# Kernel optimization log

Measured on AMD Instinct MI355X. Metric: run time of the kernel, lower is better.

The kernel has to match this reference:

```python
import jax, jax.numpy as jnp
from jax import lax
import numpy as np

INPUT_DIM = 1024; ENT_DIM = 256; KEY_DIM = 32; FUNC_DIM = 256; HID = 32
NUM_LAYERS = 1; UNIT_TYPE_DIM = 259; MAX_ENT = 64; B = 256; N = 512
NEG = 1e9

def _ln(x, g, b, eps=1e-5):
    m = x.mean(-1, keepdims=True)
    v = ((x - m) ** 2).mean(-1, keepdims=True)
    return (x - m) / jnp.sqrt(v + eps) * g + b

def setup_inputs() -> dict:
    key = jax.random.key(0)
    ks = jax.random.split(key, 16)
    def lin(k, i, o, s=0.02):
        return jax.random.normal(k, (i, o), jnp.float32) * s, jnp.zeros((o,), jnp.float32)
    p = {}
    p['key_fc_w'], p['key_fc_b'] = lin(ks[0], ENT_DIM, KEY_DIM)
    p['func_fc_w'], p['func_fc_b'] = lin(ks[1], UNIT_TYPE_DIM, FUNC_DIM)
    p['fc1_w'], p['fc1_b'] = lin(ks[2], INPUT_DIM, FUNC_DIM)
    p['fc2_w'], p['fc2_b'] = lin(ks[3], FUNC_DIM, KEY_DIM)
    p['embed_fc_w'], p['embed_fc_b'] = lin(ks[4], KEY_DIM, INPUT_DIM)
    p['lstm_wx'] = jax.random.normal(ks[5], (NUM_LAYERS, KEY_DIM, 4 * HID), jnp.float32) * 0.05
    p['lstm_wh'] = jax.random.normal(ks[6], (NUM_LAYERS, HID, 4 * HID), jnp.float32) * 0.05
    p['lstm_b'] = jnp.zeros((NUM_LAYERS, 4 * HID), jnp.float32)
    p['lstm_ln_gx'] = jnp.ones((NUM_LAYERS, 4 * HID), jnp.float32)
    p['lstm_ln_bx'] = jnp.zeros((NUM_LAYERS, 4 * HID), jnp.float32)
    p['lstm_ln_gh'] = jnp.ones((NUM_LAYERS, 4 * HID), jnp.float32)
    p['lstm_ln_bh'] = jnp.zeros((NUM_LAYERS, 4 * HID), jnp.float32)
    inp = {
        'embedding': jax.random.normal(ks[7], (B, INPUT_DIM), jnp.float32),
        'available_unit_type_mask': (jax.random.uniform(ks[8], (B, UNIT_TYPE_DIM)) < 0.5).astype(jnp.float32),
        'available_units_mask': jnp.ones((B, N), jnp.float32),
        'entity_embedding': jax.random.normal(ks[9], (B, N, ENT_DIM), jnp.float32),
        'temperature': jnp.float32(1.0),
    }
    inp.update(p)
    return inp

def reference(embedding, available_unit_type_mask, available_units_mask, entity_embedding,
              temperature, key_fc_w, key_fc_b, func_fc_w, func_fc_b, fc1_w, fc1_b,
              fc2_w, fc2_b, embed_fc_w, embed_fc_b, lstm_wx, lstm_wh, lstm_b,
              lstm_ln_gx, lstm_ln_bx, lstm_ln_gh, lstm_ln_bh):
    relu = jax.nn.relu
    # _get_key: [B,N,KEY] + end-flag row of zeros -> [B,N+1,KEY]
    key = entity_embedding @ key_fc_w + key_fc_b
    key = jnp.concatenate([key, jnp.zeros((B, 1, KEY_DIM), key.dtype)], axis=1)
    end_idx = N
    # _get_init_query
    func_embed = relu(available_unit_type_mask @ func_fc_w + func_fc_b)
    x0 = relu(embedding @ fc1_w + fc1_b)
    x0 = relu((x0 + func_embed) @ fc2_w + fc2_b)  # [B, KEY_DIM]
    mask0 = jnp.concatenate([available_units_mask, jnp.ones((B, 1), available_units_mask.dtype)], axis=1)

    h0 = jnp.zeros((NUM_LAYERS, B, HID), key.dtype)
    c0 = jnp.zeros((NUM_LAYERS, B, HID), key.dtype)
    units0 = jnp.zeros((B, N + 1), jnp.int32)
    done0 = jnp.zeros((B,), bool)
    rng0 = jax.random.key(42)

    def step(carry, _):
        x, h, c, mask, units, done, rng = carry
        xi = x
        hs, cs = [], []
        for l in range(NUM_LAYERS):  # LN-LSTM, gate order i,f,o,u (DI-engine)
            gate = (_ln(xi @ lstm_wx[l], lstm_ln_gx[l], lstm_ln_bx[l])
                    + _ln(h[l] @ lstm_wh[l], lstm_ln_gh[l], lstm_ln_bh[l]) + lstm_b[l])
            i_g, f_g, o_g, u_g = jnp.split(gate, 4, axis=-1)
            cl = jax.nn.sigmoid(f_g) * c[l] + jax.nn.sigmoid(i_g) * jnp.tanh(u_g)
            hl = jax.nn.sigmoid(o_g) * jnp.tanh(cl)
            hs.append(hl); cs.append(cl); xi = hl
        h_new = jnp.stack(hs); c_new = jnp.stack(cs)
        q = (xi[:, None, :] * key).mean(-1)          # [B, N+1] pointer scores
        q = q - (1.0 - mask) * NEG
        rng, sk = jax.random.split(rng)
        idx = jax.random.categorical(sk, q / temperature, axis=-1)  # [B]
        is_end = idx == end_idx
        active = jnp.logical_not(done)
        sel = active & jnp.logical_not(is_end)
        onehot = jax.nn.one_hot(idx, N + 1, dtype=mask.dtype)
        units = jnp.where(sel[:, None] & (onehot > 0.5), 1, units)
        mask = jnp.where(sel[:, None], mask * (1.0 - onehot), mask)
        done = done | (active & is_end)
        return (xi, h_new, c_new, mask, units, done, rng), (q, active)

    carry, (logits, valid) = lax.scan(step, (x0, h0, c0, mask0, units0, done0, rng0), None, length=MAX_ENT)
    units = carry[4]
    emb_sel = (units[..., None].astype(key.dtype) * key).mean(axis=1)  # [B, KEY_DIM]
    emb_sel = emb_sel @ embed_fc_w + embed_fc_b
    return logits, valid, units, embedding + emb_sel
```

## Files before the change

kernel.cpp:

```cpp
#include <hip/hip_runtime.h>
#include <stdint.h>
#include <stddef.h>

#define JAX_PARTITIONABLE 1

#define B_   256
#define N_   512
#define NP_  513
#define KROW 516
#define T_   64
#define CS   4
#define NCH  16
#define NEGC 1e9f

__host__ __device__ __forceinline__ void tf2x32(uint32_t k0, uint32_t k1,
    uint32_t x0, uint32_t x1, uint32_t& o0, uint32_t& o1) {
  const uint32_t k2 = k0 ^ k1 ^ 0x1BD11BDAu;
#define TFR(r) { x0 += x1; x1 = (x1 << (r)) | (x1 >> (32 - (r))); x1 ^= x0; }
  x0 += k0; x1 += k1;
  TFR(13) TFR(15) TFR(26) TFR(6)
  x0 += k1; x1 += k2 + 1u;
  TFR(17) TFR(29) TFR(16) TFR(24)
  x0 += k2; x1 += k0 + 2u;
  TFR(13) TFR(15) TFR(26) TFR(6)
// ... 1 lines not shown
  TFR(17) TFR(29) TFR(16) TFR(24)
  x0 += k1; x1 += k2 + 4u;
  TFR(13) TFR(15) TFR(26) TFR(6)
  x0 += k2; x1 += k0 + 5u;
#undef TFR
  o0 = x0; o1 = x1;
}

struct SkKeys { uint32_t k[128]; };

static SkKeys compute_chain() {
  SkKeys s;
  uint32_t r0 = 0u, r1 = 42u;
  for (int t = 0; t < 64; ++t) {
#if JAX_PARTITIONABLE
    uint32_t a0, a1, b0, b1;
    tf2x32(r0, r1, 0u, 0u, a0, a1);
    tf2x32(r0, r1, 0u, 1u, b0, b1);
    s.k[2*t] = b0; s.k[2*t+1] = b1;
    r0 = a0; r1 = a1;
#else
    uint32_t p0, p1, q0, q1;
    tf2x32(r0, r1, 0u, 2u, p0, p1);
    tf2x32(r0, r1, 1u, 3u, q0, q1);
    s.k[2*t] = p1; s.k[2*t+1] = q1;
    r0 = p0; r1 = q0;
#endif
  }
  return s;
}

__device__ __forceinline__ float gumbel_draw(uint32_t k0, uint32_t k1, int b, int n) {
  uint32_t bits;
#if JAX_PARTITIONABLE
  uint32_t j = (uint32_t)(b * NP_ + n);
  uint32_t o0, o1; tf2x32(k0, k1, 0u, j, o0, o1);
  bits = o0 ^ o1;
#else
  int j = b * NP_ + n;
  uint32_t o0, o1;
  if (j < 65664) { tf2x32(k0, k1, (uint32_t)j, (uint32_t)(j + 65664), o0, o1); bits = o0; }
  else           { tf2x32(k0, k1, (uint32_t)(j - 65664), (uint32_t)j, o0, o1); bits = o1; }
#endif
  float f = __uint_as_float((bits >> 9) | 0x3F800000u) - 1.0f;
  const float TINY = 1.17549435e-38f;
  float u = fmaxf(TINY, f + TINY);
  return -logf(-logf(u));
}

__device__ __forceinline__ float sigm(float x) {
  return 0.5f + 0.5f * tanhf(0.5f * x);
}

__device__ __forceinline__ void bar_lds() {
  asm volatile("s_waitcnt lgkmcnt(0)\n\ts_barrier" ::: "memory");
}

#define OFF_KEY   0
#define OFF_H     16512
#define OFF_Q     18560
#define OFF_G     22688
#define OFF_UNITS 33008
#define OFF_SK    33524
#define OFF_ES    33652
#define OFF_PART  33684
#define OFF_T     34196
#define OFF_X0    34452
#define LDS_FLOATS 34484

__global__ void __launch_bounds__(512, 2)
suh_fused(const float* __restrict__ emb, const float* __restrict__ autm,
          const float* __restrict__ aum, const float* __restrict__ ent,
          const float* __restrict__ temp_p,
          const float* __restrict__ key_w, const float* __restrict__ key_b,
          const float* __restrict__ func_w, const float* __restrict__ func_b,
          const float* __restrict__ fc1_w, const float* __restrict__ fc1_b,
          const float* __restrict__ fc2_w, const float* __restrict__ fc2_b,
          const float* __restrict__ emb_w, const float* __restrict__ emb_b,
          const float* __restrict__ wx, const float* __restrict__ wh,
          const float* __restrict__ lstm_bb,
          const float* __restrict__ ln_gx, const float* __restrict__ ln_bx,
          const float* __restrict__ ln_gh, const float* __restrict__ ln_bh,
          float* __restrict__ out_logits, float* __restrict__ out_valid,
          float* __restrict__ out_units, float* __restrict__ out_final,
          SkKeys sk)
{
  extern __shared__ __align__(16) float sm[];
  int* smi = (int*)sm;
  const int b   = blockIdx.x;
  const int tid = threadIdx.x;
  const int L   = tid - 64;

  const float temp = temp_p[0];

  if (tid < 256) {
    float a = 0.f;
    const float* e = emb + (size_t)b * 1024;
    #pragma unroll 8
    for (int k = 0; k < 1024; ++k) a += e[k] * fc1_w[k * 256 + tid];
    a = fmaxf(a + fc1_b[tid], 0.f);
    float f = 0.f;
    const float* m = autm + (size_t)b * 259;
    for (int k = 0; k < 259; ++k) f += m[k] * func_w[k * 256 + tid];
    f = fmaxf(f + func_b[tid], 0.f);
    sm[OFF_T + tid] = a + f;
  } else {
    if (tid < 384) smi[OFF_SK + (tid - 256)] = (int)sk.k[tid - 256];
    if (tid >= 480) sm[OFF_KEY + (tid - 480) * KROW + N_] = 0.f;
  }
  __syncthreads();

  if (tid < 32) {
    float s = 0.f;
    #pragma unroll 8
    for (int m2 = 0; m2 < 256; ++m2) s += sm[OFF_T + m2] * fc2_w[m2 * 32 + tid];
    sm[OFF_X0 + tid] = fmaxf(s + fc2_b[tid], 0.f);
  }
  __syncthreads();

  float kr0[32], kr1[32];
  float mreg[8], ureg[8];
  float m512 = 1.0f;
  int done_reg = 0;

  auto qprep = [&](int cc, int qs) {
    const int qb = OFF_Q + qs * (CS * 516);
    #pragma unroll 1
    for (int tl = 0; tl < CS; ++tl) {
      const int hb = OFF_H + (cc * CS + tl) * 32;
      float hv[32];
      #pragma unroll
      for (int r = 0; r < 8; ++r) {
        float4 v = *(const float4*)&sm[hb + r * 4];
        hv[r*4] = v.x; hv[r*4+1] = v.y; hv[r*4+2] = v.z; hv[r*4+3] = v.w;
      }
      float a0 = 0.f;
      #pragma unroll
      for (int k = 0; k < 32; ++k) a0 += hv[k] * kr0[k];
      sm[qb + tl * 516 + L] = a0 * (1.0f / 32.0f);
      if (L < 64) {
        float a1 = 0.f;
        #pragma unroll
        for (int k = 0; k < 32; ++k) a1 += hv[k] * kr1[k];
        sm[qb + tl * 516 + L + 448] = a1 * (1.0f / 32.0f);
      }
    }
  };
  auto gprep = [&](int cc, int gs) {
    const int gb = OFF_G + gs * (CS * 516);
    #pragma unroll 1
    for (int i = 0; i < 5; ++i) {
      const int idx = i * 448 + L;
      if (idx < CS * 512) {
        const int tl = idx >> 9, n = idx & 511;
        const int t = cc * CS + tl;
        sm[gb + tl * 516 + n] =
            gumbel_draw((uint32_t)smi[OFF_SK + 2*t], (uint32_t)smi[OFF_SK + 2*t + 1], b, n);
      }
    }
    if (L < CS) {
      const int t = cc * CS + L;
      sm[gb + L * 516 + N_] =
          gumbel_draw((uint32_t)smi[OFF_SK + 2*t], (uint32_t)smi[OFF_SK + 2*t + 1], b, N_);
    }
  };

  if (tid < 64) {
    float wxr0[32], wxr1[32], whr0[32], whr1[32];
    #pragma unroll
    for (int k = 0; k < 32; ++k) {
      wxr0[k] = wx[k * 128 + tid];
      wxr1[k] = wx[k * 128 + 64 + tid];
      whr0[k] = wh[k * 128 + tid];
      whr1[k] = wh[k * 128 + 64 + tid];
    }
    #pragma unroll
    for (int k = 0; k < 32; ++k) {
      asm volatile("" : "+v"(wxr0[k]), "+v"(wxr1[k]), "+v"(whr0[k]), "+v"(whr1[k]));
    }
    const float gxg0 = ln_gx[tid], gxg1 = ln_gx[tid + 64];
    const float gxb0 = ln_bx[tid], gxb1 = ln_bx[tid + 64];
    const float ghg0 = ln_gh[tid], ghg1 = ln_gh[tid + 64];
    const float ghb0 = ln_bh[tid], ghb1 = ln_bh[tid + 64];
    const float lb0  = lstm_bb[tid], lb1 = lstm_bb[tid + 64];

    float xf[32];
    #pragma unroll
    for (int r = 0; r < 8; ++r) {
      float4 v = *(const float4*)&sm[OFF_X0 + r * 4];
      xf[r*4] = v.x; xf[r*4+1] = v.y; xf[r*4+2] = v.z; xf[r*4+3] = v.w;
    }
    float creg = 0.f;

    #pragma unroll 1
    for (int t = 0; t < T_; ++t) {
      float a0 = 0.f, a1 = 0.f, b0 = 0.f, b1 = 0.f;
      #pragma unroll
      for (int k = 0; k < 32; ++k) { a0 += xf[k] * wxr0[k]; a1 += xf[k] * wxr1[k]; }
      if (t > 0) {
        #pragma unroll
        for (int k = 0; k < 32; ++k) { b0 += xf[k] * whr0[k]; b1 += xf[k] * whr1[k]; }
      }
      float sx = a0 + a1, sh = b0 + b1;
      for (int off = 32; off; off >>= 1) {
        sx += __shfl_down(sx, off);
        sh += __shfl_down(sh, off);
      }
      float mx  = __shfl(sx, 0) * (1.0f / 128.0f);
      float mh2 = __shfl(sh, 0) * (1.0f / 128.0f);
      float dx0 = a0 - mx, dx1 = a1 - mx;
      float dh0 = b0 - mh2, dh1 = b1 - mh2;
      float ssx = dx0 * dx0 + dx1 * dx1;
      float ssh = dh0 * dh0 + dh1 * dh1;
      for (int off = 32; off; off >>= 1) {
        ssx += __shfl_down(ssx, off);
        ssh += __shfl_down(ssh, off);
      }
      float vx = __shfl(ssx, 0) * (1.0f / 128.0f);
      float vh = __shfl(ssh, 0) * (1.0f / 128.0f);
      float rx = 1.0f / sqrtf(vx + 1e-5f);
      float rh = 1.0f / sqrtf(vh + 1e-5f);
      float lnx0 = dx0 * rx * gxg0 + gxb0;
      float lnx1 = dx1 * rx * gxg1 + gxb1;
      float lnh0 = dh0 * rh * ghg0 + ghb0;
      float lnh1 = dh1 * rh * ghg1 + ghb1;
      float g0 = lnx0 + lnh0 + lb0;
      float g1 = lnx1 + lnh1 + lb1;
      float fq = __shfl(g0, tid + 32);
      float uq = __shfl(g1, tid + 32);
      float cN = sigm(fq) * creg + sigm(g0) * tanhf(uq);
      float hN = sigm(g1) * tanhf(cN);
      creg = cN;
      if (tid < 32) sm[OFF_H + t * 32 + tid] = hN;
      #pragma unroll
      for (int k = 0; k < 32; ++k) xf[k] = __shfl(hN, k);
    }
  } else {
    const float4* kw4 = (const float4*)key_w;
    {
      const float4* er = (const float4*)(ent + ((size_t)b * N_ + L) * 256);
      float acc[32];
      #pragma unroll
      for (int c = 0; c < 32; ++c) acc[c] = 0.f;
      #pragma unroll 1
      for (int k4 = 0; k4 < 64; ++k4) {
        float4 ev = er[k4];
        float e4[4] = {ev.x, ev.y, ev.z, ev.w};
        #pragma unroll
        for (int j = 0; j < 4; ++j) {
          const int k = k4 * 4 + j;
          #pragma unroll
          for (int c4 = 0; c4 < 8; ++c4) {
            float4 w = kw4[k * 8 + c4];
            acc[c4*4+0] += e4[j] * w.x;
            acc[c4*4+1] += e4[j] * w.y;
            acc[c4*4+2] += e4[j] * w.z;
            acc[c4*4+3] += e4[j] * w.w;
          }
        }
      }
      #pragma unroll
      for (int c = 0; c < 32; ++c) {
        kr0[c] = acc[c] + key_b[c];
        sm[OFF_KEY + c * KROW + L] = kr0[c];
      }
    }
    if (L < 64) {
      const int n = L + 448;
      const float4* er = (const float4*)(ent + ((size_t)b * N_ + n) * 256);
      float acc[32];
      #pragma unroll
      for (int c = 0; c < 32; ++c) acc[c] = 0.f;
      #pragma unroll 1
      for (int k4 = 0; k4 < 64; ++k4) {
        float4 ev = er[k4];
        float e4[4] = {ev.x, ev.y, ev.z, ev.w};
        #pragma unroll
        for (int j = 0; j < 4; ++j) {
          const int k = k4 * 4 + j;
          #pragma unroll
          for (int c4 = 0; c4 < 8; ++c4) {
            float4 w = kw4[k * 8 + c4];
            acc[c4*4+0] += e4[j] * w.x;
            acc[c4*4+1] += e4[j] * w.y;
            acc[c4*4+2] += e4[j] * w.z;
            acc[c4*4+3] += e4[j] * w.w;
          }
        }
      }
      #pragma unroll
      for (int c = 0; c < 32; ++c) {
        kr1[c] = acc[c] + key_b[c];
        sm[OFF_KEY + c * KROW + n] = kr1[c];
      }
    }
    #pragma unroll
    for (int k = 0; k < 32; ++k) {
      asm volatile("" : "+v"(kr0[k]), "+v"(kr1[k]));
    }
    #pragma unroll 1
    for (int cc = 0; cc < 4; ++cc) gprep(cc, cc);
  }
  __syncthreads();

  if (tid < 64) {
    #pragma unroll
    for (int j = 0; j < 8; ++j) {
      mreg[j] = aum[(size_t)b * N_ + tid + 64 * j];
      ureg[j] = 0.f;
    }
  } else {
    qprep(0, 0);
  }
  bar_lds();

  for (int c = 0; c < NCH; ++c) {
    if (tid < 64) {
      const int qbase = OFF_Q + (c & 1) * (CS * 516);
      const int gbase = OFF_G + (c % 5) * (CS * 516);
      #pragma unroll 1
      for (int tl = 0; tl < CS; ++tl) {
        const int t = c * CS + tl;
        float* lrow = out_logits + ((size_t)t * B_ + b) * NP_;
        float bv = 0.f; int bi = 0;
        #pragma unroll
        for (int j = 0; j < 8; ++j) {
          const int n = tid + 64 * j;
          float q = sm[qbase + tl * 516 + n] - (1.0f - mreg[j]) * NEGC;
          lrow[n] = q;
          float v = q / temp + sm[gbase + tl * 516 + n];
          if (j == 0) { bv = v; bi = n; }
          else if (v > bv) { bv = v; bi = n; }
        }
        if (tid == 0) {
          float q = -(1.0f - m512) * NEGC;
          lrow[N_] = q;
          float v = q / temp + sm[gbase + tl * 516 + N_];
          if (v > bv) { bv = v; bi = N_; }
        }
        for (int off = 32; off; off >>= 1) {
          float ov = __shfl_down(bv, off);
          int   oi = __shfl_down(bi, off);
          if (ov > bv || (ov == bv && oi < bi)) { bv = ov; bi = oi; }
        }
        const int sel_i = __shfl(bi, 0);
        const int active = !done_reg;
        const int is_end = (sel_i == N_);
        if (tid == 0) out_valid[(size_t)t * B_ + b] = active ? 1.0f : 0.0f;
        if (active && !is_end) {
          #pragma unroll
          for (int j = 0; j < 8; ++j)
            if (tid + 64 * j == sel_i) { mreg[j] = 0.0f; ureg[j] = 1.0f; }
        }
        if (active && is_end) done_reg = 1;
      }
    } else {
      if (c + 1 < NCH) qprep(c + 1, (c + 1) & 1);
      if (c + 4 < NCH) gprep(c + 4, (c + 4) % 5);
    }
    bar_lds();
  }

  if (tid < 64) {
    #pragma unroll
    for (int j = 0; j < 8; ++j) sm[OFF_UNITS + tid + 64 * j] = ureg[j];
    if (tid == 0) sm[OFF_UNITS + N_] = 0.f;
  }
  __syncthreads();

  {
    const int g = tid >> 5, cc = tid & 31;
    float p = 0.f;
    const int n0 = g * 32;
    for (int nn = 0; nn < 32; ++nn) {
      const int n = n0 + nn;
      p += sm[OFF_UNITS + n] * sm[OFF_KEY + cc * KROW + n];
    }
    if (g == 15) p += sm[OFF_UNITS + N_] * sm[OFF_KEY + cc * KROW + N_];
    sm[OFF_PART + g * 32 + cc] = p;
  }
  for (int n = tid; n < NP_; n += 512) out_units[(size_t)b * NP_ + n] = sm[OFF_UNITS + n];
  __syncthreads();
  if (tid < 32) {
    float s = 0.f;
    #pragma unroll
    for (int g = 0; g < 16; ++g) s += sm[OFF_PART + g * 32 + tid];
    sm[OFF_ES + tid] = s / 513.0f;
  }
  __syncthreads();
  {
    const float* e = emb + (size_t)b * 1024;
    for (int d = tid; d < 1024; d += 512) {
      float a = 0.f;
      #pragma unroll
      for (int k = 0; k < 32; ++k) a += sm[OFF_ES + k] * emb_w[k * 1024 + d];
      out_final[(size_t)b * 1024 + d] = e[d] + a + emb_b[d];
    }
  }
}

extern "C" void kernel_launch(void* const* d_in, const int* in_sizes, int n_in,
                              void* d_out, int out_size, void* d_ws, size_t ws_size,
                              hipStream_t stream) {
  (void)in_sizes; (void)n_in; (void)d_ws; (void)ws_size; (void)out_size;
  const float* emb    = (const float*)d_in[0];
  const float* autm   = (const float*)d_in[1];
  const float* aum    = (const float*)d_in[2];
  const float* ent    = (const float*)d_in[3];
  const float* temp   = (const float*)d_in[4];
  const float* key_w  = (const float*)d_in[5];
  const float* key_b  = (const float*)d_in[6];
  const float* func_w = (const float*)d_in[7];
  const float* func_b = (const float*)d_in[8];
  const float* fc1_w  = (const float*)d_in[9];
  const float* fc1_b  = (const float*)d_in[10];
  const float* fc2_w  = (const float*)d_in[11];
  const float* fc2_b  = (const float*)d_in[12];
  const float* emb_w  = (const float*)d_in[13];
  const float* emb_b  = (const float*)d_in[14];
// ... 22 lines not shown
```

Baseline: 242.4 us.

## Split LSTM across two waves with LDS flags and overlap prologue work

Restructures the prologue so the LSTM recurrence is split between two wavefronts: one computes the input-side projection and gate update, the other the recurrent-side projection and layernorm, synchronised through LDS flag spin-waits. The fc1/func MLP, key projection across 256 threads, and gumbel pre-generation now run concurrently instead of in barrier-separated phases. The gumbel ring buffer shrinks from 5 to 3 slots to cut LDS use, and key rows are reloaded from LDS into registers after the barrier. This adds spin-wait handshakes per timestep and a less deep gumbel prefetch in exchange for shortening the serial prologue.

After: 246.7 us. Within noise of the previous version (+1.8%).

```diff
diff --git a/kernel.cpp b/kernel.cpp
--- a/kernel.cpp
+++ b/kernel.cpp
@@ -80,18 +80,24 @@
 __device__ __forceinline__ void bar_lds() {
   asm volatile("s_waitcnt lgkmcnt(0)\n\ts_barrier" ::: "memory");
 }
+__device__ __forceinline__ void lds_fence() {
+  asm volatile("s_waitcnt lgkmcnt(0)" ::: "memory");
+}
 
 #define OFF_KEY   0
 #define OFF_H     16512
 #define OFF_Q     18560
 #define OFF_G     22688
-#define OFF_UNITS 33008
-#define OFF_SK    33524
-#define OFF_ES    33652
-#define OFF_PART  33684
-#define OFF_T     34196
-#define OFF_X0    34452
-#define LDS_FLOATS 34484
+#define OFF_UNITS 28880
+#define OFF_LNH   29396
+#define OFF_T     29524
+#define OFF_X0    29780
+#define OFF_ES    29812
+#define OFF_PART  29844
+#define OFF_FLAGA 30356
+#define OFF_FLAGB 30420
+#define OFF_CTRT  30484
+#define LDS_FLOATS 30488
 
 __global__ void __launch_bounds__(512, 2)
 suh_fused(const float* __restrict__ emb, const float* __restrict__ autm,
@@ -112,35 +118,16 @@
 {
   extern __shared__ __align__(16) float sm[];
   int* smi = (int*)sm;
+  volatile int* vsmi = (volatile int*)sm;
   const int b   = blockIdx.x;
   const int tid = threadIdx.x;
   const int L   = tid - 64;
 
   const float temp = temp_p[0];
 
-  if (tid < 256) {
-    float a = 0.f;
-    const float* e = emb + (size_t)b * 1024;
-    #pragma unroll 8
-    for (int k = 0; k < 1024; ++k) a += e[k] * fc1_w[k * 256 + tid];
-    a = fmaxf(a + fc1_b[tid], 0.f);
-    float f = 0.f;
-    const float* m = autm + (size_t)b * 259;
-    for (int k = 0; k < 259; ++k) f += m[k] * func_w[k * 256 + tid];
-    f = fmaxf(f + func_b[tid], 0.f);
-    sm[OFF_T + tid] = a + f;
-  } else {
-    if (tid < 384) smi[OFF_SK + (tid - 256)] = (int)sk.k[tid - 256];
-    if (tid >= 480) sm[OFF_KEY + (tid - 480) * KROW + N_] = 0.f;
-  }
-  __syncthreads();
-
-  if (tid < 32) {
-    float s = 0.f;
-    #pragma unroll 8
-    for (int m2 = 0; m2 < 256; ++m2) s += sm[OFF_T + m2] * fc2_w[m2 * 32 + tid];
-    sm[OFF_X0 + tid] = fmaxf(s + fc2_b[tid], 0.f);
-  }
+  if (tid < 64)        smi[OFF_FLAGB + tid] = 0;
+  else if (tid < 128)  smi[OFF_FLAGA + (tid - 64)] = 0;
+  else if (tid == 128) smi[OFF_CTRT] = 0;
   __syncthreads();
 
   float kr0[32], kr1[32];
@@ -148,126 +135,151 @@
   float m512 = 1.0f;
   int done_reg = 0;
 
-  auto qprep = [&](int cc, int qs) {
-    const int qb = OFF_Q + qs * (CS * 516);
+  if (tid < 256) {
+    {
+      float a = 0.f;
+      const float* e = emb + (size_t)b * 1024;
+      #pragma unroll 8
+      for (int k = 0; k < 1024; ++k) a += e[k] * fc1_w[k * 256 + tid];
+      a = fmaxf(a + fc1_b[tid], 0.f);
+      float f = 0.f;
+      const float* m = autm + (size_t)b * 259;
+      for (int k = 0; k < 259; ++k) f += m[k] * func_w[k * 256 + tid];
+      f = fmaxf(f + func_b[tid], 0.f);
+      sm[OFF_T + tid] = a + f;
+    }
+    lds_fence();
+    if ((tid & 63) == 0) atomicAdd(&smi[OFF_CTRT], 1);
+
+    if (tid < 64) {
+      while (vsmi[OFF_CTRT] != 4) __builtin_amdgcn_s_sleep(1);
+      if (tid < 32) {
+        float s = 0.f;
+        #pragma unroll 8
+        for (int m2 = 0; m2 < 256; ++m2) s += sm[OFF_T + m2] * fc2_w[m2 * 32 + tid];
+        sm[OFF_X0 + tid] = fmaxf(s + fc2_b[tid], 0.f);
+      }
+      float wxr0[32], wxr1[32];
+      #pragma unroll
+      for (int k = 0; k < 32; ++k) {
+        wxr0[k] = wx[k * 128 + tid];
+        wxr1[k] = wx[k * 128 + 64 + tid];
+      }
+      #pragma unroll
+      for (int k = 0; k < 32; ++k) asm volatile("" : "+v"(wxr0[k]), "+v"(wxr1[k]));
+      const float gxg0 = ln_gx[tid], gxg1 = ln_gx[tid + 64];
+      const float gxb0 = ln_bx[tid], gxb1 = ln_bx[tid + 64];
+      const float lb0  = lstm_bb[tid], lb1 = lstm_bb[tid + 64];
+
+      float xf[32];
+      #pragma unroll
+      for (int r = 0; r < 8; ++r) {
+        float4 v = *(const float4*)&sm[OFF_X0 + r * 4];
+        xf[r*4] = v.x; xf[r*4+1] = v.y; xf[r*4+2] = v.z; xf[r*4+3] = v.w;
+      }
+      float creg = 0.f;
+
+      #pragma unroll 1
+      for (int t = 0; t < T_; ++t) {
+        float a0 = 0.f, a1 = 0.f;
+        #pragma unroll
+        for (int k = 0; k < 32; ++k) { a0 += xf[k] * wxr0[k]; a1 += xf[k] * wxr1[k]; }
+        float sx = a0 + a1;
+        for (int off = 32; off; off >>= 1) sx += __shfl_down(sx, off);
+        float mx = __shfl(sx, 0) * (1.0f / 128.0f);
+        float dx0 = a0 - mx, dx1 = a1 - mx;
+        float ssx = dx0 * dx0 + dx1 * dx1;
+        for (int off = 32; off; off >>= 1) ssx += __shfl_down(ssx, off);
+        float vx = __shfl(ssx, 0) * (1.0f / 128.0f);
+        float rx = 1.0f / sqrtf(vx + 1e-5f);
+        float lnx0 = dx0 * rx * gxg0 + gxb0;
+        float lnx1 = dx1 * rx * gxg1 + gxb1;
+        while (vsmi[OFF_FLAGA + t] == 0) __builtin_amdgcn_s_sleep(1);
+        float lnh0 = sm[OFF_LNH + tid];
+        float lnh1 = sm[OFF_LNH + 64 + tid];
+        float g0 = lnx0 + lnh0 + lb0;
+        float g1 = lnx1 + lnh1 + lb1;
+        float fq = __shfl(g0, tid + 32);
+        float uq = __shfl(g1, tid + 32);
+        float cN = sigm(fq) * creg + sigm(g0) * tanhf(uq);
+        float hN = sigm(g1) * tanhf(cN);
+        creg = cN;
+        if (tid < 32) sm[OFF_H + t * 32 + tid] = hN;
+        lds_fence();
+        if (tid == 0) smi[OFF_FLAGB + t] = 1;
+        #pragma unroll
+        for (int k = 0; k < 32; ++k) xf[k] = __shfl(hN, k);
+      }
+    } else if (tid < 128) {
+      const int l = tid - 64;
+      float whr0[32], whr1[32];
+      #pragma unroll
+      for (int k = 0; k < 32; ++k) {
+        whr0[k] = wh[k * 128 + l];
+        whr1[k] = wh[k * 128 + 64 + l];
+      }
+      #pragma unroll
+      for (int k = 0; k < 32; ++k) asm volatile("" : "+v"(whr0[k]), "+v"(whr1[k]));
+      const float ghg0 = ln_gh[l], ghg1 = ln_gh[l + 64];
+      const float ghb0 = ln_bh[l], ghb1 = ln_bh[l + 64];
+
+      #pragma unroll 1
+      for (int t = 0; t < T_; ++t) {
+        float b0 = 0.f, b1 = 0.f;
+        if (t > 0) {
+          while (vsmi[OFF_FLAGB + (t - 1)] == 0) __builtin_amdgcn_s_sleep(1);
+          float hr[32];
+          #pragma unroll
+          for (int r = 0; r < 8; ++r) {
+            float4 v = *(const float4*)&sm[OFF_H + (t - 1) * 32 + r * 4];
+            hr[r*4] = v.x; hr[r*4+1] = v.y; hr[r*4+2] = v.z; hr[r*4+3] = v.w;
+          }
+          #pragma unroll
+          for (int k = 0; k < 32; ++k) { b0 += hr[k] * whr0[k]; b1 += hr[k] * whr1[k]; }
+        }
+        float sh = b0 + b1;
+        for (int off = 32; off; off >>= 1) sh += __shfl_down(sh, off);
+        float mh2 = __shfl(sh, 0) * (1.0f / 128.0f);
+        float dh0 = b0 - mh2, dh1 = b1 - mh2;
+        float ssh = dh0 * dh0 + dh1 * dh1;
+        for (int off = 32; off; off >>= 1) ssh += __shfl_down(ssh, off);
+        float vh = __shfl(ssh, 0) * (1.0f / 128.0f);
+        float rh = 1.0f / sqrtf(vh + 1e-5f);
+        sm[OFF_LNH + l]      = dh0 * rh * ghg0 + ghb0;
+        sm[OFF_LNH + 64 + l] = dh1 * rh * ghg1 + ghb1;
+        lds_fence();
+        if (l == 0) smi[OFF_FLAGA + t] = 1;
+      }
+    } else {
+      const int L2 = tid - 128;
+      if (L2 < 32) sm[OFF_KEY + L2 * KROW + N_] = 0.f;
+      #pragma unroll 1
+      for (int cc = 0; cc < 2; ++cc) {
+        const int gb = OFF_G + cc * (CS * 516);
+        #pragma unroll 1
+        for (int ii = 0; ii < 16; ++ii) {
+          const int idx = ii * 128 + L2;
+          const int tl = idx >> 9, n = idx & 511;
+          const int t = cc * CS + tl;
+          sm[gb + tl * 516 + n] = gumbel_draw(sk.k[2*t], sk.k[2*t+1], b, n);
+        }
+        if (L2 < CS) {
+          const int t = cc * CS + L2;
+          sm[gb + L2 * 516 + N_] = gumbel_draw(sk.k[2*t], sk.k[2*t+1], b, N_);
+        }
+      }
+    }
+  } else {
+    const int i = tid - 256;
+    const float4* kw4 = (const float4*)key_w;
     #pragma unroll 1
-    for (int tl = 0; tl < CS; ++tl) {
-      const int hb = OFF_H + (cc * CS + tl) * 32;
-      float hv[32];
-      #pragma unroll
-      for (int r = 0; r < 8; ++r) {
-        float4 v = *(const float4*)&sm[hb + r * 4];
-        hv[r*4] = v.x; hv[r*4+1] = v.y; hv[r*4+2] = v.z; hv[r*4+3] = v.w;
-      }
-      float a0 = 0.f;
-      #pragma unroll
-      for (int k = 0; k < 32; ++k) a0 += hv[k] * kr0[k];
-      sm[qb + tl * 516 + L] = a0 * (1.0f / 32.0f);
-      if (L < 64) {
-        float a1 = 0.f;
-        #pragma unroll
-        for (int k = 0; k < 32; ++k) a1 += hv[k] * kr1[k];
-        sm[qb + tl * 516 + L + 448] = a1 * (1.0f / 32.0f);
-      }
-    }
-  };
-  auto gprep = [&](int cc, int gs) {
-    const int gb = OFF_G + gs * (CS * 516);
-    #pragma unroll 1
-    for (int i = 0; i < 5; ++i) {
-      const int idx = i * 448 + L;
-      if (idx < CS * 512) {
-        const int tl = idx >> 9, n = idx & 511;
-        const int t = cc * CS + tl;
-        sm[gb + tl * 516 + n] =
-            gumbel_draw((uint32_t)smi[OFF_SK + 2*t], (uint32_t)smi[OFF_SK + 2*t + 1], b, n);
-      }
-    }
-    if (L < CS) {
-      const int t = cc * CS + L;
-      sm[gb + L * 516 + N_] =
-          gumbel_draw((uint32_t)smi[OFF_SK + 2*t], (uint32_t)smi[OFF_SK + 2*t + 1], b, N_);
-    }
-  };
-
-  if (tid < 64) {
-    float wxr0[32], wxr1[32], whr0[32], whr1[32];
-    #pragma unroll
-    for (int k = 0; k < 32; ++k) {
-      wxr0[k] = wx[k * 128 + tid];
-      wxr1[k] = wx[k * 128 + 64 + tid];
-      whr0[k] = wh[k * 128 + tid];
-      whr1[k] = wh[k * 128 + 64 + tid];
-    }
-    #pragma unroll
-    for (int k = 0; k < 32; ++k) {
-      asm volatile("" : "+v"(wxr0[k]), "+v"(wxr1[k]), "+v"(whr0[k]), "+v"(whr1[k]));
-    }
-    const float gxg0 = ln_gx[tid], gxg1 = ln_gx[tid + 64];
-    const float gxb0 = ln_bx[tid], gxb1 = ln_bx[tid + 64];
-    const float ghg0 = ln_gh[tid], ghg1 = ln_gh[tid + 64];
-    const float ghb0 = ln_bh[tid], ghb1 = ln_bh[tid + 64];
-    const float lb0  = lstm_bb[tid], lb1 = lstm_bb[tid + 64];
-
-    float xf[32];
-    #pragma unroll
-    for (int r = 0; r < 8; ++r) {
-      float4 v = *(const float4*)&sm[OFF_X0 + r * 4];
-      xf[r*4] = v.x; xf[r*4+1] = v.y; xf[r*4+2] = v.z; xf[r*4+3] = v.w;
-    }
-    float creg = 0.f;
-
-    #pragma unroll 1
-    for (int t = 0; t < T_; ++t) {
-      float a0 = 0.f, a1 = 0.f, b0 = 0.f, b1 = 0.f;
-      #pragma unroll
-      for (int k = 0; k < 32; ++k) { a0 += xf[k] * wxr0[k]; a1 += xf[k] * wxr1[k]; }
-      if (t > 0) {
-        #pragma unroll
-        for (int k = 0; k < 32; ++k) { b0 += xf[k] * whr0[k]; b1 += xf[k] * whr1[k]; }
-      }
-      float sx = a0 + a1, sh = b0 + b1;
-      for (int off = 32; off; off >>= 1) {
-        sx += __shfl_down(sx, off);
-        sh += __shfl_down(sh, off);
-      }
-      float mx  = __shfl(sx, 0) * (1.0f / 128.0f);
-      float mh2 = __shfl(sh, 0) * (1.0f / 128.0f);
-      float dx0 = a0 - mx, dx1 = a1 - mx;
-      float dh0 = b0 - mh2, dh1 = b1 - mh2;
-      float ssx = dx0 * dx0 + dx1 * dx1;
-      float ssh = dh0 * dh0 + dh1 * dh1;
-      for (int off = 32; off; off >>= 1) {
-        ssx += __shfl_down(ssx, off);
-        ssh += __shfl_down(ssh, off);
-      }
-      float vx = __shfl(ssx, 0) * (1.0f / 128.0f);
-      float vh = __shfl(ssh, 0) * (1.0f / 128.0f);
-      float rx = 1.0f / sqrtf(vx + 1e-5f);
-      float rh = 1.0f / sqrtf(vh + 1e-5f);
-      float lnx0 = dx0 * rx * gxg0 + gxb0;
-      float lnx1 = dx1 * rx * gxg1 + gxb1;
-      float lnh0 = dh0 * rh * ghg0 + ghb0;
-      float lnh1 = dh1 * rh * ghg1 + ghb1;
-      float g0 = lnx0 + lnh0 + lb0;
-      float g1 = lnx1 + lnh1 + lb1;
-      float fq = __shfl(g0, tid + 32);
-      float uq = __shfl(g1, tid + 32);
-      float cN = sigm(fq) * creg + sigm(g0) * tanhf(uq);
-      float hN = sigm(g1) * tanhf(cN);
-      creg = cN;
-      if (tid < 32) sm[OFF_H + t * 32 + tid] = hN;
-      #pragma unroll
-      for (int k = 0; k < 32; ++k) xf[k] = __shfl(hN, k);
-    }
-  } else {
-    const float4* kw4 = (const float4*)key_w;
-    {
-      const float4* er = (const float4*)(ent + ((size_t)b * N_ + L) * 256);
+    for (int rnd = 0; rnd < 2; ++rnd) {
+      const int n = i + rnd * 256;
+      const float4* er = (const float4*)(ent + ((size_t)b * N_ + n) * 256);
       float acc[32];
       #pragma unroll
       for (int c = 0; c < 32; ++c) acc[c] = 0.f;
-      #pragma unroll 1
+      #pragma unroll 4
       for (int k4 = 0; k4 < 64; ++k4) {
         float4 ev = er[k4];
         float e4[4] = {ev.x, ev.y, ev.z, ev.w};
@@ -285,48 +297,51 @@
         }
       }
       #pragma unroll
-      for (int c = 0; c < 32; ++c) {
-        kr0[c] = acc[c] + key_b[c];
-        sm[OFF_KEY + c * KROW + L] = kr0[c];
-      }
-    }
-    if (L < 64) {
-      const int n = L + 448;
-      const float4* er = (const float4*)(ent + ((size_t)b * N_ + n) * 256);
-      float acc[32];
-      #pragma unroll
-      for (int c = 0; c < 32; ++c) acc[c] = 0.f;
-      #pragma unroll 1
-      for (int k4 = 0; k4 < 64; ++k4) {
-        float4 ev = er[k4];
-        float e4[4] = {ev.x, ev.y, ev.z, ev.w};
+      for (int c = 0; c < 32; ++c)
+        sm[OFF_KEY + c * KROW + n] = acc[c] + key_b[c];
+    }
+  }
+  __syncthreads();
+
+  auto qprep = [&](int cc, int qs) {
+    const int qb = OFF_Q + qs * (CS * 516);
+    #pragma unroll 1
+    for (int tl = 0; tl < CS; ++tl) {
+      const int hb = OFF_H + (cc * CS + tl) * 32;
+      float hv[32];
+      #pragma unroll
+      for (int r = 0; r < 8; ++r) {
+        float4 v = *(const float4*)&sm[hb + r * 4];
+        hv[r*4] = v.x; hv[r*4+1] = v.y; hv[r*4+2] = v.z; hv[r*4+3] = v.w;
+      }
+      float a0 = 0.f;
+      #pragma unroll
+      for (int k = 0; k < 32; ++k) a0 += hv[k] * kr0[k];
+      sm[qb + tl * 516 + L] = a0 * (1.0f / 32.0f);
+      if (L < 64) {
+        float a1 = 0.f;
         #pragma unroll
-        for (int j = 0; j < 4; ++j) {
-          const int k = k4 * 4 + j;
-          #pragma unroll
-          for (int c4 = 0; c4 < 8; ++c4) {
-            float4 w = kw4[k * 8 + c4];
-            acc[c4*4+0] += e4[j] * w.x;
-            acc[c4*4+1] += e4[j] * w.y;
-            acc[c4*4+2] += e4[j] * w.z;
-            acc[c4*4+3] += e4[j] * w.w;
-          }
-        }
-      }
-      #pragma unroll
-      for (int c = 0; c < 32; ++c) {
-        kr1[c] = acc[c] + key_b[c];
-        sm[OFF_KEY + c * KROW + n] = kr1[c];
-      }
-    }
-    #pragma unroll
-    for (int k = 0; k < 32; ++k) {
-      asm volatile("" : "+v"(kr0[k]), "+v"(kr1[k]));
-    }
+        for (int k = 0; k < 32; ++k) a1 += hv[k] * kr1[k];
+        sm[qb + tl * 516 + L + 448] = a1 * (1.0f / 32.0f);
+      }
+    }
+  };
+  auto gprep = [&](int cc, int gs) {
+    const int gb = OFF_G + gs * (CS * 516);
     #pragma unroll 1
-    for (int cc = 0; cc < 4; ++cc) gprep(cc, cc);
-  }
-  __syncthreads();
+    for (int ii = 0; ii < 5; ++ii) {
+      const int idx = ii * 448 + L;
+      if (idx < CS * 512) {
+        const int tl = idx >> 9, n = idx & 511;
+        const int t = cc * CS + tl;
+        sm[gb + tl * 516 + n] = gumbel_draw(sk.k[2*t], sk.k[2*t+1], b, n);
+      }
+    }
+    if (L < CS) {
+      const int t = cc * CS + L;
+      sm[gb + L * 516 + N_] = gumbel_draw(sk.k[2*t], sk.k[2*t+1], b, N_);
+    }
+  };
 
   if (tid < 64) {
     #pragma unroll
@@ -335,6 +350,12 @@
       ureg[j] = 0.f;
     }
   } else {
+    #pragma unroll
+    for (int c = 0; c < 32; ++c) kr0[c] = sm[OFF_KEY + c * KROW + L];
+    if (L < 65) {
+      #pragma unroll
+      for (int c = 0; c < 32; ++c) kr1[c] = sm[OFF_KEY + c * KROW + L + 448];
+    }
     qprep(0, 0);
   }
   bar_lds();
@@ -342,7 +363,7 @@
   for (int c = 0; c < NCH; ++c) {
     if (tid < 64) {
       const int qbase = OFF_Q + (c & 1) * (CS * 516);
-      const int gbase = OFF_G + (c % 5) * (CS * 516);
+      const int gbase = OFF_G + (c % 3) * (CS * 516);
       #pragma unroll 1
       for (int tl = 0; tl < CS; ++tl) {
         const int t = c * CS + tl;
@@ -381,7 +402,7 @@
       }
     } else {
       if (c + 1 < NCH) qprep(c + 1, (c + 1) & 1);
-      if (c + 4 < NCH) gprep(c + 4, (c + 4) % 5);
+      if (c + 2 < NCH) gprep(c + 2, (c + 2) % 3);
     }
     bar_lds();
   }
```

## Replace block barriers with per-wave LDS flag pipeline across specialized waves

Applied to the files above, without the earlier changes.

Block-wide barriers in the chunked sampling loop are replaced by LDS flags and counters, so each wave runs as an independent producer or consumer. The wavefronts are assigned fixed roles: LSTM recurrence, gumbel generation, the sampling consumer, and q-score computation from the key in LDS. The LSTM wave now publishes h per step and runs ahead while the other waves consume it. The LSTM weights move from registers to LDS, and key computation is split across four waves that overlap the fc1 prologue. The change relies on spin-waits over volatile LDS, which risks memory-ordering bugs, and LDS use grows, which may limit occupancy.

Measured after the change: 305.8 us. 1.26x slower.

```diff
diff --git a/kernel.cpp b/kernel.cpp
--- a/kernel.cpp
+++ b/kernel.cpp
@@ -77,21 +77,28 @@
   return 0.5f + 0.5f * tanhf(0.5f * x);
 }
 
-__device__ __forceinline__ void bar_lds() {
-  asm volatile("s_waitcnt lgkmcnt(0)\n\ts_barrier" ::: "memory");
+__device__ __forceinline__ void lds_fence() {
+  asm volatile("s_waitcnt lgkmcnt(0)" ::: "memory");
 }
 
 #define OFF_KEY   0
 #define OFF_H     16512
-#define OFF_Q     18560
-#define OFF_G     22688
-#define OFF_UNITS 33008
-#define OFF_SK    33524
-#define OFF_ES    33652
-#define OFF_PART  33684
-#define OFF_T     34196
-#define OFF_X0    34452
-#define LDS_FLOATS 34484
+#define OFF_WB    18560
+#define OFF_Q     26752
+#define OFF_G     30880
+#define OFF_UNITS 37072
+#define OFF_T     37588
+#define OFF_X0    37844
+#define OFF_ES    37876
+#define OFF_PART  37908
+#define OFF_SK    38420
+#define OFF_FLAGB 38548
+#define OFF_QCNT  38612
+#define OFF_GRDY  38628
+#define OFF_SPROG 38644
+#define OFF_KEYC  38645
+#define OFF_CTRT  38646
+#define LDS_FLOATS 38648
 
 __global__ void __launch_bounds__(512, 2)
 suh_fused(const float* __restrict__ emb, const float* __restrict__ autm,
@@ -112,11 +119,27 @@
 {
   extern __shared__ __align__(16) float sm[];
   int* smi = (int*)sm;
-  const int b   = blockIdx.x;
-  const int tid = threadIdx.x;
-  const int L   = tid - 64;
+  volatile int* vsmi = (volatile int*)sm;
+  const int b    = blockIdx.x;
+  const int tid  = threadIdx.x;
+  const int lane = tid & 63;
 
   const float temp = temp_p[0];
+
+  {
+    const float4* wx4 = (const float4*)wx;
+    const float4* wh4 = (const float4*)wh;
+    float4* wb4 = (float4*)(sm + OFF_WB);
+    for (int i = tid; i < 1024; i += 512) wb4[i] = wx4[i];
+    for (int i = tid; i < 1024; i += 512) wb4[1024 + i] = wh4[i];
+    if (tid < 64)        smi[OFF_FLAGB + tid] = 0;
+    else if (tid < 80)   smi[OFF_QCNT + (tid - 64)] = 0;
+    else if (tid < 96)   smi[OFF_GRDY + (tid - 80)] = 0;
+    else if (tid == 96)  { smi[OFF_SPROG] = 0; smi[OFF_KEYC] = 0; smi[OFF_CTRT] = 0; }
+    else if (tid >= 128 && tid < 256) smi[OFF_SK + tid - 128] = (int)sk.k[tid - 128];
+    else if (tid >= 448 && tid < 480) sm[OFF_KEY + (tid - 448) * KROW + N_] = 0.f;
+  }
+  __syncthreads();
 
   if (tid < 256) {
     float a = 0.f;
@@ -129,79 +152,68 @@
     for (int k = 0; k < 259; ++k) f += m[k] * func_w[k * 256 + tid];
     f = fmaxf(f + func_b[tid], 0.f);
     sm[OFF_T + tid] = a + f;
+    lds_fence();
+    if (lane == 0) atomicAdd(&smi[OFF_CTRT], 1);
   } else {
-    if (tid < 384) smi[OFF_SK + (tid - 256)] = (int)sk.k[tid - 256];
-    if (tid >= 480) sm[OFF_KEY + (tid - 480) * KROW + N_] = 0.f;
-  }
-  __syncthreads();
-
-  if (tid < 32) {
-    float s = 0.f;
-    #pragma unroll 8
-    for (int m2 = 0; m2 < 256; ++m2) s += sm[OFF_T + m2] * fc2_w[m2 * 32 + tid];
-    sm[OFF_X0 + tid] = fmaxf(s + fc2_b[tid], 0.f);
-  }
-  __syncthreads();
-
-  float kr0[32], kr1[32];
-  float mreg[8], ureg[8];
-  float m512 = 1.0f;
-  int done_reg = 0;
-
-  auto qprep = [&](int cc, int qs) {
-    const int qb = OFF_Q + qs * (CS * 516);
+    const int i = tid - 256;
+    const float4* kw4 = (const float4*)key_w;
+    #pragma unroll 1
+    for (int rnd = 0; rnd < 2; ++rnd) {
+      const int n = i + rnd * 256;
+      const float4* er = (const float4*)(ent + ((size_t)b * N_ + n) * 256);
+      float acc[32];
+      #pragma unroll
+      for (int c = 0; c < 32; ++c) acc[c] = 0.f;
+      #pragma unroll 4
+      for (int k4 = 0; k4 < 64; ++k4) {
+        float4 ev = er[k4];
+        float e4[4] = {ev.x, ev.y, ev.z, ev.w};
+        #pragma unroll
+        for (int j = 0; j < 4; ++j) {
+          const int k = k4 * 4 + j;
+          #pragma unroll
+          for (int c4 = 0; c4 < 8; ++c4) {
+            float4 w = kw4[k * 8 + c4];
+            acc[c4*4+0] += e4[j] * w.x;
+            acc[c4*4+1] += e4[j] * w.y;
+            acc[c4*4+2] += e4[j] * w.z;
+            acc[c4*4+3] += e4[j] * w.w;
+          }
+        }
+      }
+      #pragma unroll
+      for (int c = 0; c < 32; ++c)
+        sm[OFF_KEY + c * KROW + n] = acc[c] + key_b[c];
+    }
+    lds_fence();
+    if (lane == 0) atomicAdd(&smi[OFF_KEYC], 1);
+  }
+
+  auto gchunk = [&](int c) {
+    if (c >= 3) while (vsmi[OFF_SPROG] < c - 2) __builtin_amdgcn_s_sleep(1);
+    const int gb = OFF_G + (c % 3) * 2064;
     #pragma unroll 1
     for (int tl = 0; tl < CS; ++tl) {
-      const int hb = OFF_H + (cc * CS + tl) * 32;
-      float hv[32];
-      #pragma unroll
-      for (int r = 0; r < 8; ++r) {
-        float4 v = *(const float4*)&sm[hb + r * 4];
-        hv[r*4] = v.x; hv[r*4+1] = v.y; hv[r*4+2] = v.z; hv[r*4+3] = v.w;
-      }
-      float a0 = 0.f;
-      #pragma unroll
-      for (int k = 0; k < 32; ++k) a0 += hv[k] * kr0[k];
-      sm[qb + tl * 516 + L] = a0 * (1.0f / 32.0f);
-      if (L < 64) {
-        float a1 = 0.f;
-        #pragma unroll
-        for (int k = 0; k < 32; ++k) a1 += hv[k] * kr1[k];
-        sm[qb + tl * 516 + L + 448] = a1 * (1.0f / 32.0f);
-      }
-    }
+      const int t = c * CS + tl;
+      const uint32_t k0 = (uint32_t)smi[OFF_SK + 2 * t];
+      const uint32_t k1 = (uint32_t)smi[OFF_SK + 2 * t + 1];
+      #pragma unroll 1
+      for (int it = 0; it < 9; ++it) {
+        const int n = it * 64 + lane;
+        if (n < NP_) sm[gb + tl * 516 + n] = gumbel_draw(k0, k1, b, n);
+      }
+    }
+    lds_fence();
+    if (lane == 0) vsmi[OFF_GRDY + c] = 1;
   };
-  auto gprep = [&](int cc, int gs) {
-    const int gb = OFF_G + gs * (CS * 516);
-    #pragma unroll 1
-    for (int i = 0; i < 5; ++i) {
-      const int idx = i * 448 + L;
-      if (idx < CS * 512) {
-        const int tl = idx >> 9, n = idx & 511;
-        const int t = cc * CS + tl;
-        sm[gb + tl * 516 + n] =
-            gumbel_draw((uint32_t)smi[OFF_SK + 2*t], (uint32_t)smi[OFF_SK + 2*t + 1], b, n);
-      }
-    }
-    if (L < CS) {
-      const int t = cc * CS + L;
-      sm[gb + L * 516 + N_] =
-          gumbel_draw((uint32_t)smi[OFF_SK + 2*t], (uint32_t)smi[OFF_SK + 2*t + 1], b, N_);
-    }
-  };
 
   if (tid < 64) {
-    float wxr0[32], wxr1[32], whr0[32], whr1[32];
-    #pragma unroll
-    for (int k = 0; k < 32; ++k) {
-      wxr0[k] = wx[k * 128 + tid];
-      wxr1[k] = wx[k * 128 + 64 + tid];
-      whr0[k] = wh[k * 128 + tid];
-      whr1[k] = wh[k * 128 + 64 + tid];
-    }
-    #pragma unroll
-    for (int k = 0; k < 32; ++k) {
-      asm volatile("" : "+v"(wxr0[k]), "+v"(wxr1[k]), "+v"(whr0[k]), "+v"(whr1[k]));
+    while (vsmi[OFF_CTRT] != 4) __builtin_amdgcn_s_sleep(1);
+    if (tid < 32) {
+      float s = 0.f;
+      #pragma unroll 8
+      for (int m2 = 0; m2 < 256; ++m2) s += sm[OFF_T + m2] * fc2_w[m2 * 32 + tid];
+      sm[OFF_X0 + tid] = fmaxf(s + fc2_b[tid], 0.f);
     }
     const float gxg0 = ln_gx[tid], gxg1 = ln_gx[tid + 64];
     const float gxb0 = ln_bx[tid], gxb1 = ln_bx[tid + 64];
@@ -221,10 +233,16 @@
     for (int t = 0; t < T_; ++t) {
       float a0 = 0.f, a1 = 0.f, b0 = 0.f, b1 = 0.f;
       #pragma unroll
-      for (int k = 0; k < 32; ++k) { a0 += xf[k] * wxr0[k]; a1 += xf[k] * wxr1[k]; }
+      for (int k = 0; k < 32; ++k) {
+        a0 += xf[k] * sm[OFF_WB + k * 128 + tid];
+        a1 += xf[k] * sm[OFF_WB + k * 128 + 64 + tid];
+      }
       if (t > 0) {
         #pragma unroll
-        for (int k = 0; k < 32; ++k) { b0 += xf[k] * whr0[k]; b1 += xf[k] * whr1[k]; }
+        for (int k = 0; k < 32; ++k) {
+          b0 += xf[k] * sm[OFF_WB + 4096 + k * 128 + tid];
+          b1 += xf[k] * sm[OFF_WB + 4096 + k * 128 + 64 + tid];
+        }
       }
       float sx = a0 + a1, sh = b0 + b1;
       for (int off = 32; off; off >>= 1) {
@@ -257,92 +275,27 @@
       float hN = sigm(g1) * tanhf(cN);
       creg = cN;
       if (tid < 32) sm[OFF_H + t * 32 + tid] = hN;
+      lds_fence();
+      if (tid == 0) vsmi[OFF_FLAGB + t] = 1;
       #pragma unroll
       for (int k = 0; k < 32; ++k) xf[k] = __shfl(hN, k);
     }
-  } else {
-    const float4* kw4 = (const float4*)key_w;
-    {
-      const float4* er = (const float4*)(ent + ((size_t)b * N_ + L) * 256);
-      float acc[32];
-      #pragma unroll
-      for (int c = 0; c < 32; ++c) acc[c] = 0.f;
-      #pragma unroll 1
-      for (int k4 = 0; k4 < 64; ++k4) {
-        float4 ev = er[k4];
-        float e4[4] = {ev.x, ev.y, ev.z, ev.w};
-        #pragma unroll
-        for (int j = 0; j < 4; ++j) {
-          const int k = k4 * 4 + j;
-          #pragma unroll
-          for (int c4 = 0; c4 < 8; ++c4) {
-            float4 w = kw4[k * 8 + c4];
-            acc[c4*4+0] += e4[j] * w.x;
-            acc[c4*4+1] += e4[j] * w.y;
-            acc[c4*4+2] += e4[j] * w.z;
-            acc[c4*4+3] += e4[j] * w.w;
-          }
-        }
-      }
-      #pragma unroll
-      for (int c = 0; c < 32; ++c) {
-        kr0[c] = acc[c] + key_b[c];
-        sm[OFF_KEY + c * KROW + L] = kr0[c];
-      }
-    }
-    if (L < 64) {
-      const int n = L + 448;
-      const float4* er = (const float4*)(ent + ((size_t)b * N_ + n) * 256);
-      float acc[32];
-      #pragma unroll
-      for (int c = 0; c < 32; ++c) acc[c] = 0.f;
-      #pragma unroll 1
-      for (int k4 = 0; k4 < 64; ++k4) {
-        float4 ev = er[k4];
-        float e4[4] = {ev.x, ev.y, ev.z, ev.w};
-        #pragma unroll
-        for (int j = 0; j < 4; ++j) {
-          const int k = k4 * 4 + j;
-          #pragma unroll
-          for (int c4 = 0; c4 < 8; ++c4) {
-            float4 w = kw4[k * 8 + c4];
-            acc[c4*4+0] += e4[j] * w.x;
-            acc[c4*4+1] += e4[j] * w.y;
-            acc[c4*4+2] += e4[j] * w.z;
-            acc[c4*4+3] += e4[j] * w.w;
-          }
-        }
-      }
-      #pragma unroll
-      for (int c = 0; c < 32; ++c) {
-        kr1[c] = acc[c] + key_b[c];
-        sm[OFF_KEY + c * KROW + n] = kr1[c];
-      }
-    }
-    #pragma unroll
-    for (int k = 0; k < 32; ++k) {
-      asm volatile("" : "+v"(kr0[k]), "+v"(kr1[k]));
-    }
-    #pragma unroll 1
-    for (int cc = 0; cc < 4; ++cc) gprep(cc, cc);
-  }
-  __syncthreads();
-
-  if (tid < 64) {
+  } else if (tid < 128) {
+    gchunk(0); gchunk(2);
+  } else if (tid < 192) {
+    float mreg[8], ureg[8];
     #pragma unroll
     for (int j = 0; j < 8; ++j) {
-      mreg[j] = aum[(size_t)b * N_ + tid + 64 * j];
+      mreg[j] = aum[(size_t)b * N_ + lane + 64 * j];
       ureg[j] = 0.f;
     }
-  } else {
-    qprep(0, 0);
-  }
-  bar_lds();
-
-  for (int c = 0; c < NCH; ++c) {
-    if (tid < 64) {
-      const int qbase = OFF_Q + (c & 1) * (CS * 516);
-      const int gbase = OFF_G + (c % 5) * (CS * 516);
+    float m512 = 1.0f;
+    int done_reg = 0;
+    for (int c = 0; c < NCH; ++c) {
+      while (!(vsmi[OFF_QCNT + c] == 2 && vsmi[OFF_GRDY + c] == 1))
+        __builtin_amdgcn_s_sleep(1);
+      const int qbase = OFF_Q + (c & 1) * 2064;
+      const int gbase = OFF_G + (c % 3) * 2064;
       #pragma unroll 1
       for (int tl = 0; tl < CS; ++tl) {
         const int t = c * CS + tl;
@@ -350,14 +303,14 @@
         float bv = 0.f; int bi = 0;
         #pragma unroll
         for (int j = 0; j < 8; ++j) {
-          const int n = tid + 64 * j;
+          const int n = lane + 64 * j;
           float q = sm[qbase + tl * 516 + n] - (1.0f - mreg[j]) * NEGC;
           lrow[n] = q;
           float v = q / temp + sm[gbase + tl * 516 + n];
           if (j == 0) { bv = v; bi = n; }
           else if (v > bv) { bv = v; bi = n; }
         }
-        if (tid == 0) {
+        if (lane == 0) {
           float q = -(1.0f - m512) * NEGC;
           lrow[N_] = q;
           float v = q / temp + sm[gbase + tl * 516 + N_];
@@ -371,25 +324,54 @@
         const int sel_i = __shfl(bi, 0);
         const int active = !done_reg;
         const int is_end = (sel_i == N_);
-        if (tid == 0) out_valid[(size_t)t * B_ + b] = active ? 1.0f : 0.0f;
+        if (lane == 0) out_valid[(size_t)t * B_ + b] = active ? 1.0f : 0.0f;
         if (active && !is_end) {
           #pragma unroll
           for (int j = 0; j < 8; ++j)
-            if (tid + 64 * j == sel_i) { mreg[j] = 0.0f; ureg[j] = 1.0f; }
+            if (lane + 64 * j == sel_i) { mreg[j] = 0.0f; ureg[j] = 1.0f; }
         }
         if (active && is_end) done_reg = 1;
       }
-    } else {
-      if (c + 1 < NCH) qprep(c + 1, (c + 1) & 1);
-      if (c + 4 < NCH) gprep(c + 4, (c + 4) % 5);
-    }
-    bar_lds();
-  }
-
-  if (tid < 64) {
+      lds_fence();
+      if (lane == 0) vsmi[OFF_SPROG] = c + 1;
+    }
     #pragma unroll
-    for (int j = 0; j < 8; ++j) sm[OFF_UNITS + tid + 64 * j] = ureg[j];
-    if (tid == 0) sm[OFF_UNITS + N_] = 0.f;
+    for (int j = 0; j < 8; ++j) sm[OFF_UNITS + lane + 64 * j] = ureg[j];
+    if (lane == 0) sm[OFF_UNITS + N_] = 0.f;
+  } else if (tid < 256) {
+    gchunk(1); gchunk(3);
+  } else if (tid < 320) {
+    for (int c = 4; c < NCH; c += 2) gchunk(c);
+  } else if (tid < 384) {
+    for (int c = 5; c < NCH; c += 2) gchunk(c);
+  } else {
+    const int j = tid - 384;
+    while (vsmi[OFF_KEYC] != 4) __builtin_amdgcn_s_sleep(1);
+    for (int c = 0; c < NCH; ++c) {
+      if (c >= 1) while (vsmi[OFF_SPROG] < c - 1) __builtin_amdgcn_s_sleep(1);
+      while (vsmi[OFF_FLAGB + 4 * c + 3] == 0) __builtin_amdgcn_s_sleep(1);
+      const int qb = OFF_Q + (c & 1) * 2064;
+      #pragma unroll 1
+      for (int tl = 0; tl < CS; ++tl) {
+        const int hb = OFF_H + (c * CS + tl) * 32;
+        float hv[32];
+        #pragma unroll
+        for (int r = 0; r < 8; ++r) {
+          float4 v = *(const float4*)&sm[hb + r * 4];
+          hv[r*4] = v.x; hv[r*4+1] = v.y; hv[r*4+2] = v.z; hv[r*4+3] = v.w;
+        }
+        #pragma unroll
+        for (int r = 0; r < 4; ++r) {
+          const int n = j + r * 128;
+          float acc = 0.f;
+          #pragma unroll
+          for (int k = 0; k < 32; ++k) acc += hv[k] * sm[OFF_KEY + k * KROW + n];
+          sm[qb + tl * 516 + n] = acc * (1.0f / 32.0f);
+        }
+      }
+      lds_fence();
+      if (lane == 0) atomicAdd(&smi[OFF_QCNT + c], 1);
+    }
   }
   __syncthreads();
 
```

## Stage LSTM weights in LDS and shrink gumbel prefetch ring to cut registers

Applied to the files above, without the earlier changes.

Moves the LSTM input and hidden weight matrices from 128 per-thread registers into shared memory, and replaces the shuffle broadcast of h with LDS vector reads. The gumbel prefetch ring shrinks from five chunks to three, so fewer chunks are drawn before the main loop. The key-projection loop is now partially unrolled. The aim is to relieve register pressure under the 512x2 launch bounds and shorten the prologue, at the cost of extra LDS reads on the serial LSTM critical path.

Result: slower. 378.6 us (+56.2%).

```diff
diff --git a/kernel.cpp b/kernel.cpp
--- a/kernel.cpp
+++ b/kernel.cpp
@@ -80,18 +80,22 @@
 __device__ __forceinline__ void bar_lds() {
   asm volatile("s_waitcnt lgkmcnt(0)\n\ts_barrier" ::: "memory");
 }
+__device__ __forceinline__ void lds_fence() {
+  asm volatile("s_waitcnt lgkmcnt(0)" ::: "memory");
+}
 
 #define OFF_KEY   0
 #define OFF_H     16512
-#define OFF_Q     18560
-#define OFF_G     22688
-#define OFF_UNITS 33008
-#define OFF_SK    33524
-#define OFF_ES    33652
-#define OFF_PART  33684
-#define OFF_T     34196
-#define OFF_X0    34452
-#define LDS_FLOATS 34484
+#define OFF_WB    18560
+#define OFF_Q     26752
+#define OFF_G     30880
+#define OFF_UNITS 37072
+#define OFF_SK    37588
+#define OFF_ES    37716
+#define OFF_PART  37748
+#define OFF_T     38260
+#define OFF_X0    38516
+#define LDS_FLOATS 38548
 
 __global__ void __launch_bounds__(512, 2)
 suh_fused(const float* __restrict__ emb, const float* __restrict__ autm,
@@ -118,6 +122,17 @@
 
   const float temp = temp_p[0];
 
+  {
+    const float4* wx4 = (const float4*)wx;
+    const float4* wh4 = (const float4*)wh;
+    float4* wb4 = (float4*)(sm + OFF_WB);
+    for (int i = tid; i < 1024; i += 512) wb4[i] = wx4[i];
+    for (int i = tid; i < 1024; i += 512) wb4[1024 + i] = wh4[i];
+    if (tid < 128) smi[OFF_SK + tid] = (int)sk.k[tid];
+    if (tid >= 480) sm[OFF_KEY + (tid - 480) * KROW + N_] = 0.f;
+  }
+  __syncthreads();
+
   if (tid < 256) {
     float a = 0.f;
     const float* e = emb + (size_t)b * 1024;
@@ -129,9 +144,6 @@
     for (int k = 0; k < 259; ++k) f += m[k] * func_w[k * 256 + tid];
     f = fmaxf(f + func_b[tid], 0.f);
     sm[OFF_T + tid] = a + f;
-  } else {
-    if (tid < 384) smi[OFF_SK + (tid - 256)] = (int)sk.k[tid - 256];
-    if (tid >= 480) sm[OFF_KEY + (tid - 480) * KROW + N_] = 0.f;
   }
   __syncthreads();
 
@@ -174,8 +186,8 @@
   auto gprep = [&](int cc, int gs) {
     const int gb = OFF_G + gs * (CS * 516);
     #pragma unroll 1
-    for (int i = 0; i < 5; ++i) {
-      const int idx = i * 448 + L;
+    for (int ii = 0; ii < 5; ++ii) {
+      const int idx = ii * 448 + L;
       if (idx < CS * 512) {
         const int tl = idx >> 9, n = idx & 511;
         const int t = cc * CS + tl;
@@ -191,18 +203,6 @@
   };
 
   if (tid < 64) {
-    float wxr0[32], wxr1[32], whr0[32], whr1[32];
-    #pragma unroll
-    for (int k = 0; k < 32; ++k) {
-      wxr0[k] = wx[k * 128 + tid];
-      wxr1[k] = wx[k * 128 + 64 + tid];
-      whr0[k] = wh[k * 128 + tid];
-      whr1[k] = wh[k * 128 + 64 + tid];
-    }
-    #pragma unroll
-    for (int k = 0; k < 32; ++k) {
-      asm volatile("" : "+v"(wxr0[k]), "+v"(wxr1[k]), "+v"(whr0[k]), "+v"(whr1[k]));
-    }
     const float gxg0 = ln_gx[tid], gxg1 = ln_gx[tid + 64];
     const float gxb0 = ln_bx[tid], gxb1 = ln_bx[tid + 64];
     const float ghg0 = ln_gh[tid], ghg1 = ln_gh[tid + 64];
@@ -221,10 +221,16 @@
     for (int t = 0; t < T_; ++t) {
       float a0 = 0.f, a1 = 0.f, b0 = 0.f, b1 = 0.f;
       #pragma unroll
-      for (int k = 0; k < 32; ++k) { a0 += xf[k] * wxr0[k]; a1 += xf[k] * wxr1[k]; }
+      for (int k = 0; k < 32; ++k) {
+        a0 += xf[k] * sm[OFF_WB + k * 128 + tid];
+        a1 += xf[k] * sm[OFF_WB + k * 128 + 64 + tid];
+      }
       if (t > 0) {
         #pragma unroll
-        for (int k = 0; k < 32; ++k) { b0 += xf[k] * whr0[k]; b1 += xf[k] * whr1[k]; }
+        for (int k = 0; k < 32; ++k) {
+          b0 += xf[k] * sm[OFF_WB + 4096 + k * 128 + tid];
+          b1 += xf[k] * sm[OFF_WB + 4096 + k * 128 + 64 + tid];
+        }
       }
       float sx = a0 + a1, sh = b0 + b1;
       for (int off = 32; off; off >>= 1) {
@@ -257,8 +263,12 @@
       float hN = sigm(g1) * tanhf(cN);
       creg = cN;
       if (tid < 32) sm[OFF_H + t * 32 + tid] = hN;
-      #pragma unroll
-      for (int k = 0; k < 32; ++k) xf[k] = __shfl(hN, k);
+      lds_fence();
+      #pragma unroll
+      for (int r = 0; r < 8; ++r) {
+        float4 v = *(const float4*)&sm[OFF_H + t * 32 + r * 4];
+        xf[r*4] = v.x; xf[r*4+1] = v.y; xf[r*4+2] = v.z; xf[r*4+3] = v.w;
+      }
     }
   } else {
     const float4* kw4 = (const float4*)key_w;
@@ -267,7 +277,7 @@
       float acc[32];
       #pragma unroll
       for (int c = 0; c < 32; ++c) acc[c] = 0.f;
-      #pragma unroll 1
+      #pragma unroll 4
       for (int k4 = 0; k4 < 64; ++k4) {
         float4 ev = er[k4];
         float e4[4] = {ev.x, ev.y, ev.z, ev.w};
@@ -296,7 +306,7 @@
       float acc[32];
       #pragma unroll
       for (int c = 0; c < 32; ++c) acc[c] = 0.f;
-      #pragma unroll 1
+      #pragma unroll 4
       for (int k4 = 0; k4 < 64; ++k4) {
         float4 ev = er[k4];
         float e4[4] = {ev.x, ev.y, ev.z, ev.w};
@@ -323,8 +333,8 @@
     for (int k = 0; k < 32; ++k) {
       asm volatile("" : "+v"(kr0[k]), "+v"(kr1[k]));
     }
-    #pragma unroll 1
-    for (int cc = 0; cc < 4; ++cc) gprep(cc, cc);
+    gprep(0, 0);
+    gprep(1, 1);
   }
   __syncthreads();
 
@@ -342,7 +352,7 @@
   for (int c = 0; c < NCH; ++c) {
     if (tid < 64) {
       const int qbase = OFF_Q + (c & 1) * (CS * 516);
-      const int gbase = OFF_G + (c % 5) * (CS * 516);
+      const int gbase = OFF_G + (c % 3) * (CS * 516);
       #pragma unroll 1
       for (int tl = 0; tl < CS; ++tl) {
         const int t = c * CS + tl;
@@ -381,7 +391,7 @@
       }
     } else {
       if (c + 1 < NCH) qprep(c + 1, (c + 1) & 1);
-      if (c + 4 < NCH) gprep(c + 4, (c + 4) % 5);
+      if (c + 2 < NCH) gprep(c + 2, (c + 2) % 3);
     }
     bar_lds();
   }
```
